# Kernel tuning notes

Measured on AMD Instinct MI355X. Metric: run time of the kernel, lower is better.

The kernel has to match this reference:

```python
import jax, jax.numpy as jnp
import numpy as np

D = 1024
H = 16
HD = D // H
EPS = 1e-6


def rms_norm(x, w):
    # x: [..., hd]; compute in float32 like the torch module
    xf = x.astype(jnp.float32)
    rms = jnp.sqrt(jnp.mean(xf * xf, axis=-1, keepdims=True) + EPS)
    return (xf / rms * w.astype(jnp.float32)).astype(x.dtype)


def setup_inputs() -> dict:
    key = jax.random.key(0)
    ks = jax.random.split(key, 6)
    B, S = 2, 2048
    x = jax.random.normal(ks[0], (B, S, D), dtype=jnp.float32)
    Wqkv = jax.random.normal(ks[1], (3 * D, D), dtype=jnp.float32) * (1.0 / np.sqrt(D))
    bqkv = jax.random.normal(ks[2], (3 * D,), dtype=jnp.float32) * 0.02
    Wproj = jax.random.normal(ks[3], (D, D), dtype=jnp.float32) * (1.0 / np.sqrt(D))
    bproj = jax.random.normal(ks[4], (D,), dtype=jnp.float32) * 0.02
    qn_w = jnp.ones((HD,), dtype=jnp.float32)
    kn_w = jnp.ones((HD,), dtype=jnp.float32)
    return {"x": x, "Wqkv": Wqkv, "bqkv": bqkv, "Wproj": Wproj, "bproj": bproj,
            "qn_w": qn_w, "kn_w": kn_w}


def reference(x, Wqkv, bqkv, Wproj, bproj, qn_w, kn_w):
    B, S, _ = x.shape
    # QKV projection: torch Linear is x @ W.T + b
    qkv = x @ Wqkv.T + bqkv                     # [B, S, 3D]
    qkv = qkv.reshape(B, S, 3, H, HD)
    q, k, v = qkv[:, :, 0], qkv[:, :, 1], qkv[:, :, 2]   # each [B, S, H, hd]
    q = rms_norm(q, qn_w)
    k = rms_norm(k, kn_w)
    # move heads forward: [B, H, S, hd]
    q = q.transpose(0, 2, 1, 3)
    k = k.transpose(0, 2, 1, 3)
    v = v.transpose(0, 2, 1, 3)
    scale = 1.0 / np.sqrt(HD)
    scores = jnp.einsum('bhsd,bhtd->bhst', q, k) * scale   # [B, H, S, S] (math backend)
    attn = jax.nn.softmax(scores, axis=-1)
    out = jnp.einsum('bhst,bhtd->bhsd', attn, v)            # [B, H, S, hd]
    out = out.transpose(0, 2, 1, 3).reshape(B, S, D)
    return out @ Wproj.T + bproj
```

## Files before the change

kernel.cpp:

```cpp
#include <hip/hip_runtime.h>
#include <hip/hip_bf16.h>
#include <math.h>

#define D_MODEL 1024
#define NH 16
#define HD 64
#define SEQ 2048
#define BATCH 2
#define NTOK (BATCH*SEQ)

typedef short bf16x8 __attribute__((ext_vector_type(8)));
typedef short s4 __attribute__((ext_vector_type(4)));
typedef float f32x4 __attribute__((ext_vector_type(4)));
typedef unsigned short us4 __attribute__((ext_vector_type(4)));

#define MFMA(a,b,c) __builtin_amdgcn_mfma_f32_16x16x32_bf16(a,b,c,0,0,0)

union bfu { __hip_bfloat16 b; unsigned short u; };
__device__ __forceinline__ unsigned short f2b(float f){ bfu t; t.b = __float2bfloat16(f); return t.u; }
__device__ __forceinline__ float b2f(unsigned short u){ bfu t; t.u = u; return __bfloat162float(t.b); }
__device__ __forceinline__ unsigned short f2bf(float f){
    unsigned int u = __float_as_uint(f);
    u += 0x7FFFu + ((u >> 16) & 1u);
    return (unsigned short)(u >> 16);
}

__device__ __forceinline__ void g2l16(const unsigned short* g, unsigned short* l){
    __builtin_amdgcn_global_load_lds(
        (const __attribute__((address_space(1))) unsigned int*)g,
        (__attribute__((address_space(3))) unsigned int*)l, 16, 0, 0);
}

#define OFF_X   128L
#define OFF_WQ  (OFF_X  + 4194304L)
#define OFF_BQ  (OFF_WQ + 3145728L)
#define OFF_WP  (OFF_BQ + 3072L)
#define OFF_BP  (OFF_WP + 1048576L)
#define OFF_QN  (OFF_BP + 1024L)
#define OFF_KN  (OFF_QN + 64L)
#define OFF_Q   (OFF_KN + 64L)
#define OFF_K   (OFF_Q  + 4194304L)
#define OFF_V   (OFF_K  + 4194304L)
#define OFF_A   (OFF_V  + 4194304L)


__global__ __launch_bounds__(256) void detect_kernel(
    const unsigned int* __restrict__ xraw, int* __restrict__ cnt)
{
    int i = blockIdx.x*256 + threadIdx.x;
    uint4 v = ((const uint4*)xraw)[i];
    unsigned int w[4] = {v.x, v.y, v.z, v.w};
    int local = 0;
    #pragma unroll
    for (int j=0;j<4;j++){
        local += ((w[j] & 0x7F80u) >= 0x4800u);
        local += (((w[j]>>16) & 0x7F80u) >= 0x4800u);
    }
    if (local) atomicAdd(cnt, local);
}

__global__ __launch_bounds__(256) void convert_kernel(
    const void* __restrict__ x,  const void* __restrict__ wq,
    const void* __restrict__ bq, const void* __restrict__ wp,
    const void* __restrict__ bp, const void* __restrict__ qn,
    const void* __restrict__ kn, unsigned short* __restrict__ ws,
    const int* __restrict__ cntp)
{
    const int flag = (*cntp > 256);
    long i = (long)blockIdx.x*blockDim.x + threadIdx.x;
    const long stride = (long)gridDim.x*blockDim.x;
    const long NCH = 2098208L;
    for (; i < NCH; i += stride){
        long j = i; const void* src; long off;
        if (j < 1048576L)                  { src = x;  off = OFF_X;  }
        else if ((j -= 1048576L) < 786432L){ src = wq; off = OFF_WQ; }
        else if ((j -= 786432L)  < 768L)   { src = bq; off = OFF_BQ; }
        else if ((j -= 768L)     < 262144L){ src = wp; off = OFF_WP; }
        else if ((j -= 262144L)  < 256L)   { src = bp; off = OFF_BP; }
        else if ((j -= 256L)     < 16L)    { src = qn; off = OFF_QN; }
        else      { j -= 16L;                src = kn; off = OFF_KN; }
        us4 o;
        if (flag){
            float4 v = ((const float4*)src)[j];
            o.x = f2b(v.x); o.y = f2b(v.y); o.z = f2b(v.z); o.w = f2b(v.w);
        } else {
            o = ((const us4*)src)[j];
        }
        *(us4*)(ws + off + j*4) = o;
    }
}

__global__ __launch_bounds__(256) void qkv_kernel(
    const unsigned short* __restrict__ x,
    const unsigned short* __restrict__ Wqkv,
    const unsigned short* __restrict__ bqkv,
    const unsigned short* __restrict__ qn_w,
    const unsigned short* __restrict__ kn_w,
    unsigned short* __restrict__ qbuf,
    unsigned short* __restrict__ kbuf,
    unsigned short* __restrict__ vbuf)
{
    __shared__ __align__(16) unsigned short tA0[128*32];
    __shared__ __align__(16) unsigned short tA1[128*32];
    __shared__ __align__(16) unsigned short tB0[128*32];
    __shared__ __align__(16) unsigned short tB1[128*32];
    const int tid  = threadIdx.x;
    const int w    = tid >> 6, lane = tid & 63, quad = lane >> 4, c = lane & 15;
    const int m0 = blockIdx.y*128, n0 = blockIdx.x*128;
    const int am = (w>>1)*64, bn = (w&1)*64;
    const int kq = quad ^ ((c>>1)&3);

    f32x4 acc[4][4];
    for (int mi=0;mi<4;mi++) for (int ni=0;ni<4;ni++) acc[mi][ni] = {0.f,0.f,0.f,0.f};

    const int i0 = tid, i1 = tid + 256;
    const int r0 = i0>>2, cc0 = (i0&3) ^ ((r0>>1)&3);
    const int r1 = i1>>2, cc1 = (i1&3) ^ ((r1>>1)&3);
    const long gaA0 = (long)(m0 + r0)*D_MODEL + cc0*8;
    const long gaA1 = (long)(m0 + r1)*D_MODEL + cc1*8;
    const long gbB0 = (long)(n0 + r0)*D_MODEL + cc0*8;
    const long gbB1 = (long)(n0 + r1)*D_MODEL + cc1*8;

#define QKV_STAGE(BUFA, BUFB, T) do{ const int kk_ = (T)*32; \
    g2l16(x    + gaA0 + kk_, BUFA + i0*8); \
    g2l16(x    + gaA1 + kk_, BUFA + i1*8); \
    g2l16(Wqkv + gbB0 + kk_, BUFB + i0*8); \
    g2l16(Wqkv + gbB1 + kk_, BUFB + i1*8); }while(0)

#define QKV_COMP(BUFA, BUFB) do{ \
    bf16x8 a_[4], b_[4]; \
    _Pragma("unroll") \
    for (int mi=0;mi<4;mi++) \
        a_[mi] = *(const bf16x8*)(BUFA + ((am + mi*16 + c)*4 + kq)*8); \
    _Pragma("unroll") \
    for (int ni=0;ni<4;ni++) \
        b_[ni] = *(const bf16x8*)(BUFB + ((bn + ni*16 + c)*4 + kq)*8); \
    _Pragma("unroll") \
    for (int mi=0;mi<4;mi++) \
        _Pragma("unroll") \
        for (int ni=0;ni<4;ni++) \
            acc[mi][ni] = MFMA(a_[mi], b_[ni], acc[mi][ni]); }while(0)

    QKV_STAGE(tA0, tB0, 0);
    __syncthreads();

    for (int t=0; t<32; t+=2){
        QKV_STAGE(tA1, tB1, t+1);
        QKV_COMP(tA0, tB0);
        __syncthreads();
        if (t+2 < 32) QKV_STAGE(tA0, tB0, t+2);
        QKV_COMP(tA1, tB1);
        __syncthreads();
    }
#undef QKV_STAGE
#undef QKV_COMP

    const int nw = n0 + bn, mw = m0 + am;
    const int region = nw >> 10;
    const int h      = (nw & 1023) >> 6;
    float bias[4], wn[4];
    for (int ni=0;ni<4;ni++){
        bias[ni] = b2f(bqkv[nw + ni*16 + c]);
        wn[ni]   = 1.0f;
    }
    if (region==0) for (int ni=0;ni<4;ni++) wn[ni] = b2f(qn_w[ni*16+c]) * 0.18033688f;
    if (region==1) for (int ni=0;ni<4;ni++) wn[ni] = b2f(kn_w[ni*16+c]);

    for (int mi=0;mi<4;mi++){
        for (int ni=0;ni<4;ni++)
            for (int r=0;r<4;r++) acc[mi][ni][r] += bias[ni];

        float scale_r[4];
        if (region < 2){
            for (int r=0;r<4;r++){
                float ss = 0.f;
                for (int ni=0;ni<4;ni++){ float v2 = acc[mi][ni][r]; ss += v2*v2; }
                ss += __shfl_xor(ss, 1, 64);
                ss += __shfl_xor(ss, 2, 64);
                ss += __shfl_xor(ss, 4, 64);
                ss += __shfl_xor(ss, 8, 64);
                scale_r[r] = rsqrtf(ss*(1.0f/64.0f) + 1e-6f);
            }
        } else {
            for (int r=0;r<4;r++) scale_r[r] = 1.0f;
        }

        for (int r=0;r<4;r++){
            int m = mw + mi*16 + quad*4 + r;
            int bidx = m >> 11, s = m & 2047;
            long bb = (long)(bidx*NH + h)*SEQ*HD;
            if (region == 0){
                long base = bb + (long)s*HD;
                for (int ni=0;ni<4;ni++)
                    qbuf[base + ni*16 + c] = f2bf(acc[mi][ni][r] * scale_r[r] * wn[ni]);
            } else if (region == 1){
                long tb = bb + (long)(s>>6)*4096;
                for (int ni=0;ni<4;ni++){
                    int d = ni*16 + c;
                    long idx = tb + (long)((s&63)*8 + ((d>>3) ^ (s&7)))*8 + (d&7);
                    kbuf[idx] = f2bf(acc[mi][ni][r] * scale_r[r] * wn[ni]);
                }
            } else {
                long tb = bb + (long)(s>>6)*4096;
                int ch2  = (s>>4)&3;
                int fb   = ((s>>2)&3)*4;
                int mloc = s&3;
                for (int ni=0;ni<4;ni++){
                    int d = ni*16 + c;
                    int f = fb + (((d>>1) + ch2)&3);
                    long idx = tb + (long)d*64 + f*4 + mloc;
                    vbuf[idx] = f2bf(acc[mi][ni][r]);
                }
            }
        }
    }
}

__global__ __launch_bounds__(256, 4) void attn_kernel(
    const unsigned short* __restrict__ qbuf,
    const unsigned short* __restrict__ kts,
    const unsigned short* __restrict__ vts,
    unsigned short* __restrict__ abuf)
{
    const int tid = threadIdx.x, w = tid>>6, lane = tid&63, quad = lane>>4, c = lane&15;
    const int bh = blockIdx.y, qt = blockIdx.x;
    const unsigned short* qb = qbuf + (long)bh*SEQ*HD;
    const unsigned short* kb = kts + (long)bh*SEQ*HD;
    const unsigned short* vb = vts + (long)bh*SEQ*HD;
    const int qbase = qt*64 + w*16;
    const int cq = c & 7;

    __shared__ __align__(16) unsigned short KT0[4096];
    __shared__ __align__(16) unsigned short KT1[4096];
    __shared__ __align__(16) unsigned short VT0[4096];
    __shared__ __align__(16) unsigned short VT1[4096];

    bf16x8 aq[2];
    #pragma unroll
    for (int ks=0;ks<2;ks++)
        aq[ks] = *(const bf16x8*)(qb + (long)(qbase + c)*HD + ks*32 + quad*8);

    f32x4 o[4];
    #pragma unroll
    for (int nt=0;nt<4;nt++) o[nt] = {0.f,0.f,0.f,0.f};
    f32x4 l4 = {0.f,0.f,0.f,0.f};

#define STAGE2(SRC, DST) do{ \
    g2l16((SRC) + tid*8,        DST + tid*8); \
    g2l16((SRC) + 2048 + tid*8, DST + 2048 + tid*8); }while(0)

#define ATTN_TILE(KTB, VTB) do{ \
    bf16x8 kf_[4][2]; \
    _Pragma("unroll") \
    for (int mt=0;mt<4;mt++) \
        _Pragma("unroll") \
        for (int ks=0;ks<2;ks++) \
            kf_[mt][ks] = *(const bf16x8*)(KTB + ((mt*16+c)*8 + ((ks*4+quad)^cq))*8); \
    f32x4 z4_[4]; \
    _Pragma("unroll") \
    for (int mt=0;mt<4;mt++){ \
        f32x4 t_ = {0.f,0.f,0.f,0.f}; \
        t_ = MFMA(kf_[mt][0], aq[0], t_); \
        t_ = MFMA(kf_[mt][1], aq[1], t_); \
        z4_[mt] = t_; \
    } \
    unsigned int pk_[4][2]; \
    _Pragma("unroll") \
    for (int mt=0;mt<4;mt++){ \
        float p0 = __builtin_amdgcn_exp2f(z4_[mt][0]); \
        float p1 = __builtin_amdgcn_exp2f(z4_[mt][1]); \
        float p2 = __builtin_amdgcn_exp2f(z4_[mt][2]); \
        float p3 = __builtin_amdgcn_exp2f(z4_[mt][3]); \
        l4[0] += p0; l4[1] += p1; l4[2] += p2; l4[3] += p3; \
        pk_[mt][0] = __builtin_amdgcn_perm(__float_as_uint(p1), __float_as_uint(p0), 0x07060302u); \
        pk_[mt][1] = __builtin_amdgcn_perm(__float_as_uint(p3), __float_as_uint(p2), 0x07060302u); \
    } \
    _Pragma("unroll") \
    for (int ks=0;ks<2;ks++){ \
        union { unsigned int u[4]; bf16x8 v; } pB_; \
        pB_.u[0] = pk_[2*ks][0];   pB_.u[1] = pk_[2*ks][1]; \
        pB_.u[2] = pk_[2*ks+1][0]; pB_.u[3] = pk_[2*ks+1][1]; \
        _Pragma("unroll") \
        for (int nt=0;nt<4;nt++){ \
            const int dv_ = nt*16 + c; \
            const unsigned short* vbase_ = VTB + dv_*64; \
            int flo_ = quad*4 + (((dv_>>1) + ks*2    )&3); \
            int fhi_ = quad*4 + (((dv_>>1) + ks*2 + 1)&3); \
            uint2 lo_ = *(const uint2*)(vbase_ + flo_*4); \
            uint2 hi_ = *(const uint2*)(vbase_ + fhi_*4); \
            union { unsigned int u[4]; bf16x8 v; } vv_; \
            vv_.u[0]=lo_.x; vv_.u[1]=lo_.y; vv_.u[2]=hi_.x; vv_.u[3]=hi_.y; \
            o[nt] = MFMA(vv_.v, pB_.v, o[nt]); \
        } \
    } }while(0)

    STAGE2(kb, KT0); STAGE2(vb, VT0);
    __syncthreads();

    for (int kt2=0; kt2<SEQ/64; kt2+=2){
        STAGE2(kb + (kt2+1)*4096, KT1);
        STAGE2(vb + (kt2+1)*4096, VT1);
        ATTN_TILE(KT0, VT0);
        __syncthreads();
        if (kt2+2 < SEQ/64){
            STAGE2(kb + (kt2+2)*4096, KT0);
            STAGE2(vb + (kt2+2)*4096, VT0);
        }
        ATTN_TILE(KT1, VT1);
        __syncthreads();
    }
#undef STAGE2
#undef ATTN_TILE

    float l_loc = (l4[0]+l4[1]) + (l4[2]+l4[3]);
    l_loc += __shfl_xor(l_loc, 16, 64);
    l_loc += __shfl_xor(l_loc, 32, 64);
    float inv = 1.0f / l_loc;

    const int b = bh >> 4, h = bh & 15;
    long base = ((long)(b*SEQ + qbase + c)*NH + h)*HD;
    #pragma unroll
    for (int nt=0;nt<4;nt++){
        us4 pkd;
        #pragma unroll
        for (int r=0;r<4;r++) pkd[r] = f2bf(o[nt][r]*inv);
        *(us4*)(abuf + base + nt*16 + quad*4) = pkd;
    }
}

__global__ __launch_bounds__(256) void proj_kernel(
    const unsigned short* __restrict__ abuf,
    const unsigned short* __restrict__ Wp,
    const unsigned short* __restrict__ bp,
    void* __restrict__ outv,
    const int* __restrict__ cntp)
{
    __shared__ __align__(16) unsigned short tA0[128*32];
    __shared__ __align__(16) unsigned short tA1[128*32];
    __shared__ __align__(16) unsigned short tB0[64*32];
    __shared__ __align__(16) unsigned short tB1[64*32];
    const int tid  = threadIdx.x;
    const int w    = tid >> 6, lane = tid & 63, quad = lane >> 4, c = lane & 15;
    const int m0 = blockIdx.y*128, n0 = blockIdx.x*64;
    const int am = (w>>1)*64, bn = (w&1)*32;
    const int kq = quad ^ ((c>>1)&3);
    const int flag = (*cntp > 256);

    f32x4 acc[4][2];
    for (int mi=0;mi<4;mi++) for (int ni=0;ni<2;ni++) acc[mi][ni] = {0.f,0.f,0.f,0.f};

    const int i0 = tid, i1 = tid + 256;
    const int r0 = i0>>2, cc0 = (i0&3) ^ ((r0>>1)&3);
    const int r1 = i1>>2, cc1 = (i1&3) ^ ((r1>>1)&3);
    const long gaA0 = (long)(m0 + r0)*D_MODEL + cc0*8;
    const long gaA1 = (long)(m0 + r1)*D_MODEL + cc1*8;
    const long gbB0 = (long)(n0 + r0)*D_MODEL + cc0*8;

#define PROJ_STAGE(BUFA, BUFB, T) do{ const int kk_ = (T)*32; \
    g2l16(abuf + gaA0 + kk_, BUFA + i0*8); \
    g2l16(abuf + gaA1 + kk_, BUFA + i1*8); \
    g2l16(Wp   + gbB0 + kk_, BUFB + i0*8); }while(0)

#define PROJ_COMP(BUFA, BUFB) do{ \
    bf16x8 a_[4], b_[2]; \
    _Pragma("unroll") \
    for (int mi=0;mi<4;mi++) \
        a_[mi] = *(const bf16x8*)(BUFA + ((am + mi*16 + c)*4 + kq)*8); \
    _Pragma("unroll") \
    for (int ni=0;ni<2;ni++) \
        b_[ni] = *(const bf16x8*)(BUFB + ((bn + ni*16 + c)*4 + kq)*8); \
    _Pragma("unroll") \
    for (int mi=0;mi<4;mi++) \
        _Pragma("unroll") \
        for (int ni=0;ni<2;ni++) \
            acc[mi][ni] = MFMA(a_[mi], b_[ni], acc[mi][ni]); }while(0)

    PROJ_STAGE(tA0, tB0, 0);
    __syncthreads();

    for (int t=0; t<32; t+=2){
        PROJ_STAGE(tA1, tB1, t+1);
        PROJ_COMP(tA0, tB0);
        __syncthreads();
        if (t+2 < 32) PROJ_STAGE(tA0, tB0, t+2);
        PROJ_COMP(tA1, tB1);
        __syncthreads();
    }
#undef PROJ_STAGE
#undef PROJ_COMP

    float bias[2];
    for (int ni=0;ni<2;ni++) bias[ni] = b2f(bp[n0 + bn + ni*16 + c]);

    for (int mi=0;mi<4;mi++)
        for (int r=0;r<4;r++){
            long m = m0 + am + mi*16 + quad*4 + r;
            for (int ni=0;ni<2;ni++){
                float val = acc[mi][ni][r] + bias[ni];
                long idx = m*D_MODEL + n0 + bn + ni*16 + c;
                if (flag) ((float*)outv)[idx] = val;
                else      ((unsigned short*)outv)[idx] = f2bf(val);
            }
        }
}

extern "C" void kernel_launch(void* const* d_in, const int* in_sizes, int n_in,
                              void* d_out, int out_size, void* d_ws, size_t ws_size,
                              hipStream_t stream)
{
    unsigned short* ws = (unsigned short*)d_ws;
    int* cnt = (int*)d_ws;

    hipMemsetAsync(cnt, 0, 4, stream);
    hipLaunchKernelGGL(detect_kernel, dim3(16), dim3(256), 0, stream,
                       (const unsigned int*)d_in[0], cnt);
    hipLaunchKernelGGL(convert_kernel, dim3(2048), dim3(256), 0, stream,
                       d_in[0], d_in[1], d_in[2], d_in[3], d_in[4], d_in[5], d_in[6],
                       ws, cnt);
    hipLaunchKernelGGL(qkv_kernel,  dim3(24,32), dim3(256), 0, stream,
                       ws+OFF_X, ws+OFF_WQ, ws+OFF_BQ, ws+OFF_QN, ws+OFF_KN,
                       ws+OFF_Q, ws+OFF_K, ws+OFF_V);
    hipLaunchKernelGGL(attn_kernel, dim3(32,32), dim3(256), 0, stream,
                       ws+OFF_Q, ws+OFF_K, ws+OFF_V, ws+OFF_A);
    hipLaunchKernelGGL(proj_kernel, dim3(16,32), dim3(256), 0, stream,
                       ws+OFF_A, ws+OFF_WP, ws+OFF_BP, d_out, cnt);
}
```

Before: 213.7 us.

## Use partial vmcnt waits to keep two LDS stages in flight in GEMMs

The QKV and output-projection GEMM main loops now prefetch two stages ahead. They replace __syncthreads (a full vmcnt(0) drain) with s_waitcnt vmcnt(N) plus a raw s_barrier, so the next tile's global-to-LDS loads stay in flight while the current tile is computed. Scheduling barriers keep the compiler from reordering loads across these points. The aim is to hide global load latency that the full drain used to expose, at the cost of depending on exact vmcnt accounting to stay correct.

```diff
diff --git a/kernel.cpp b/kernel.cpp
--- a/kernel.cpp
+++ b/kernel.cpp
@@ -30,6 +30,9 @@
         (const __attribute__((address_space(1))) unsigned int*)g,
         (__attribute__((address_space(3))) unsigned int*)l, 16, 0, 0);
 }
+
+#define WAITVM(N) asm volatile("s_waitcnt vmcnt(" #N ")" ::: "memory")
+#define RBAR do{ __builtin_amdgcn_s_barrier(); __builtin_amdgcn_sched_barrier(0); }while(0)
 
 #define OFF_X   128L
 #define OFF_WQ  (OFF_X  + 4194304L)
@@ -125,7 +128,8 @@
     g2l16(x    + gaA0 + kk_, BUFA + i0*8); \
     g2l16(x    + gaA1 + kk_, BUFA + i1*8); \
     g2l16(Wqkv + gbB0 + kk_, BUFB + i0*8); \
-    g2l16(Wqkv + gbB1 + kk_, BUFB + i1*8); }while(0)
+    g2l16(Wqkv + gbB1 + kk_, BUFB + i1*8); \
+    __builtin_amdgcn_sched_barrier(0); }while(0)
 
 #define QKV_COMP(BUFA, BUFB) do{ \
     bf16x8 a_[4], b_[4]; \
@@ -142,16 +146,22 @@
             acc[mi][ni] = MFMA(a_[mi], b_[ni], acc[mi][ni]); }while(0)
 
     QKV_STAGE(tA0, tB0, 0);
-    __syncthreads();
-
-    for (int t=0; t<32; t+=2){
-        QKV_STAGE(tA1, tB1, t+1);
+    QKV_STAGE(tA1, tB1, 1);
+
+    for (int t=0; t<30; t+=2){
+        WAITVM(4); RBAR;
         QKV_COMP(tA0, tB0);
-        __syncthreads();
-        if (t+2 < 32) QKV_STAGE(tA0, tB0, t+2);
+        RBAR;
+        QKV_STAGE(tA0, tB0, t+2);
+        WAITVM(4); RBAR;
         QKV_COMP(tA1, tB1);
-        __syncthreads();
-    }
+        RBAR;
+        QKV_STAGE(tA1, tB1, t+3);
+    }
+    WAITVM(4); RBAR;
+    QKV_COMP(tA0, tB0);
+    WAITVM(0); RBAR;
+    QKV_COMP(tA1, tB1);
 #undef QKV_STAGE
 #undef QKV_COMP
 
@@ -359,7 +369,8 @@
 #define PROJ_STAGE(BUFA, BUFB, T) do{ const int kk_ = (T)*32; \
     g2l16(abuf + gaA0 + kk_, BUFA + i0*8); \
     g2l16(abuf + gaA1 + kk_, BUFA + i1*8); \
-    g2l16(Wp   + gbB0 + kk_, BUFB + i0*8); }while(0)
+    g2l16(Wp   + gbB0 + kk_, BUFB + i0*8); \
+    __builtin_amdgcn_sched_barrier(0); }while(0)
 
 #define PROJ_COMP(BUFA, BUFB) do{ \
     bf16x8 a_[4], b_[2]; \
@@ -376,16 +387,22 @@
             acc[mi][ni] = MFMA(a_[mi], b_[ni], acc[mi][ni]); }while(0)
 
     PROJ_STAGE(tA0, tB0, 0);
-    __syncthreads();
-
-    for (int t=0; t<32; t+=2){
-        PROJ_STAGE(tA1, tB1, t+1);
+    PROJ_STAGE(tA1, tB1, 1);
+
+    for (int t=0; t<30; t+=2){
+        WAITVM(3); RBAR;
         PROJ_COMP(tA0, tB0);
-        __syncthreads();
-        if (t+2 < 32) PROJ_STAGE(tA0, tB0, t+2);
+        RBAR;
+        PROJ_STAGE(tA0, tB0, t+2);
+        WAITVM(3); RBAR;
         PROJ_COMP(tA1, tB1);
-        __syncthreads();
-    }
+        RBAR;
+        PROJ_STAGE(tA1, tB1, t+3);
+    }
+    WAITVM(3); RBAR;
+    PROJ_COMP(tA0, tB0);
+    WAITVM(0); RBAR;
+    PROJ_COMP(tA1, tB1);
 #undef PROJ_STAGE
 #undef PROJ_COMP
 
```

Measured after the change: 215.9 us. Within noise of the previous version (+1.0%).
